# Performance work log

Hardware: AMD Instinct MI355X
Metric: run time of the kernel (lower is better)

## Reference

```python
import jax, jax.numpy as jnp
import numpy as np
from jax import lax

B, S, D, E, H = 2, 2048, 1024, 8, 4096


def setup_inputs() -> dict:
    key = jax.random.key(0)
    ks = jax.random.split(key, 10)
    sc = 0.02  # GPT-style init scale
    return {
        "x": jax.random.normal(ks[0], (B, S, D), jnp.float32),
        "noise": jax.random.normal(ks[1], (B, S, E), jnp.float32),
        "w_route": jax.random.normal(ks[2], (D, E), jnp.float32) * sc,
        "b_route": jnp.zeros((E,), jnp.float32),
        "w_noise": jax.random.normal(ks[3], (D, E), jnp.float32) * sc,
        "b_noise": jnp.zeros((E,), jnp.float32),
        "w_fc": jax.random.normal(ks[4], (E, D, H), jnp.float32) * sc,
        "b_fc": jnp.zeros((E, H), jnp.float32),
        "w_proj": jax.random.normal(ks[5], (E, H, D), jnp.float32) * sc,
        "b_proj": jnp.zeros((E, D), jnp.float32),
        "top_k": 2,
    }


def reference(x, noise, w_route, b_route, w_noise, b_noise, w_fc, b_fc, w_proj, b_proj, top_k):
    # --- NoisyTopkRouter ---
    logits = x @ w_route + b_route                      # [B,S,E]
    noise_logits = x @ w_noise + b_noise                # [B,S,E]
    noisy = logits + noise * jax.nn.softplus(noise_logits)
    gate1 = jax.nn.softmax(noisy, axis=-1)              # dense gate (aux output)

    topk_vals, topk_idx = lax.top_k(noisy, top_k)       # [B,S,K]
    # softmax over sparse logits (-inf elsewhere) == softmax over the top-k values
    gk = jax.nn.softmax(topk_vals, axis=-1)             # [B,S,K]
    # scatter top-k gates back to the dense expert axis; non-selected experts get 0
    gating = (jax.nn.one_hot(topk_idx, E, dtype=x.dtype) * gk[..., None]).sum(-2)  # [B,S,E]

    # --- Experts (dense-over-experts, masked by gating; math identical to
    #     masked gather/scatter since non-selected gates are exactly 0) ---
    h = jnp.einsum('bsd,edh->bseh', x, w_fc) + b_fc     # [B,S,E,H]
    h = jax.nn.gelu(h, approximate=True)                # GELU(tanh)
    y = jnp.einsum('bseh,ehd->bsed', h, w_proj) + b_proj  # [B,S,E,D]
    out = jnp.einsum('bsed,bse->bsd', y, gating)        # weighted combine
    return out, gate1
```

## Files before the change

### kernel.cpp

```cpp
#include <hip/hip_runtime.h>
#include <cstdint>


#define DEV __device__ __forceinline__

typedef __attribute__((ext_vector_type(8))) short short8;
typedef __attribute__((ext_vector_type(4))) float floatx4;

constexpr int D_ = 1024, E_ = 8, H_ = 4096;
constexpr int NTOK = 4096;
constexpr int CAP  = 4096;
constexpr int TOTSLOT = NTOK * 2;

constexpr size_t O_COUNT = 0;
constexpr size_t O_FLAG  = 48;
constexpr size_t O_OFFS  = 64;
constexpr size_t O_BTOK  = 128;
constexpr size_t O_BGATE = O_BTOK  + (size_t)E_ * CAP * 4;
constexpr size_t O_PAIR  = O_BGATE + (size_t)E_ * CAP * 4;
constexpr size_t O_HBUF  = (O_PAIR + (size_t)NTOK * 2 * 4 + 255) & ~(size_t)255;
constexpr size_t O_YBUF  = O_HBUF + (size_t)TOTSLOT * H_ * 2;
constexpr size_t WS_NEED = O_YBUF + (size_t)TOTSLOT * D_ * 2;

DEV float b2f(unsigned short u) {
    union { unsigned int i; float f; } v; v.i = ((unsigned int)u) << 16; return v.f;
}
DEV unsigned int f2b(float f) {
    union { float f; unsigned int i; } v; v.f = f;
    unsigned int r = v.i + 0x7fffu + ((v.i >> 16) & 1u);
    return (r >> 16) & 0xffffu;
}

template <int DT> DEV float ldf(const void* p, size_t i) {
    if constexpr (DT == 0) return ((const float*)p)[i];
    else return b2f(((const unsigned short*)p)[i]);
}

DEV float gelu_tanh(float x) {
    float u = 0.7978845608028654f * (x + 0.044715f * x * x * x);
    u = fminf(fmaxf(u, -20.f), 20.f);
    float e = __expf(2.f * u);
    float t = (e - 1.f) / (e + 1.f);
    return 0.5f * x * (1.f + t);
}

__global__ __launch_bounds__(64) void detect_init(const unsigned int* __restrict__ xw,
                                                  int* flags, int* counts) {
    int lane = threadIdx.x;
    int outl = 0;
    for (int i = lane; i < 512; i += 64) {
        unsigned int lo = xw[i] & 0xffffu;
        unsigned int ef = (lo >> 7) & 0xffu;
        if (ef < 100u || ef > 140u) outl++;
    }
#pragma unroll
    for (int off = 32; off > 0; off >>= 1) outl += __shfl_down(outl, off);
    if (lane == 0) flags[0] = (outl > 64) ? 0 : 1;
    if (lane < E_) counts[lane] = 0;
}

template <int DT>
__global__ __launch_bounds__(256) void router_kernel(
    const void* __restrict__ x, const void* __restrict__ noise,
    const void* __restrict__ w_route, const void* __restrict__ b_route,
    const void* __restrict__ w_noise, const void* __restrict__ b_noise,
    void* __restrict__ out,
    const int* __restrict__ flags, int* counts, int* btok, float* bgate, int* pairs)
{
    if (flags[0] != DT) return;
    int wave = threadIdx.x >> 6, lane = threadIdx.x & 63;
    int t = blockIdx.x * 4 + wave;

    double racc[E_], nacc[E_];
#pragma unroll
    for (int e = 0; e < E_; e++) { racc[e] = 0.0; nacc[e] = 0.0; }

#pragma unroll 4
    for (int i = 0; i < D_ / 64; i++) {
        int j = i * 64 + lane;
        float xv = ldf<DT>(x, (size_t)t * D_ + j);
        float rv[E_], nv[E_];
        if constexpr (DT == 0) {
            const float* wr = (const float*)w_route + (size_t)j * E_;
            const float* wn = (const float*)w_noise + (size_t)j * E_;
            float4 a0 = ((const float4*)wr)[0], a1 = ((const float4*)wr)[1];
            float4 c0 = ((const float4*)wn)[0], c1 = ((const float4*)wn)[1];
            rv[0]=a0.x; rv[1]=a0.y; rv[2]=a0.z; rv[3]=a0.w;
            rv[4]=a1.x; rv[5]=a1.y; rv[6]=a1.z; rv[7]=a1.w;
            nv[0]=c0.x; nv[1]=c0.y; nv[2]=c0.z; nv[3]=c0.w;
            nv[4]=c1.x; nv[5]=c1.y; nv[6]=c1.z; nv[7]=c1.w;
        } else {
            uint4 r8 = *(const uint4*)((const unsigned short*)w_route + (size_t)j * E_);
            uint4 n8 = *(const uint4*)((const unsigned short*)w_noise + (size_t)j * E_);
            const unsigned int rw[4] = {r8.x, r8.y, r8.z, r8.w};
            const unsigned int nw[4] = {n8.x, n8.y, n8.z, n8.w};
#pragma unroll
            for (int p = 0; p < 4; p++) {
                rv[2*p]   = b2f((unsigned short)(rw[p] & 0xffffu));
                rv[2*p+1] = b2f((unsigned short)(rw[p] >> 16));
                nv[2*p]   = b2f((unsigned short)(nw[p] & 0xffffu));
                nv[2*p+1] = b2f((unsigned short)(nw[p] >> 16));
            }
        }
#pragma unroll
        for (int e = 0; e < E_; e++) {
            racc[e] += (double)(xv * rv[e]);
            nacc[e] += (double)(xv * nv[e]);
        }
    }
#pragma unroll
    for (int off = 32; off > 0; off >>= 1)
#pragma unroll
        for (int e = 0; e < E_; e++) {
            racc[e] += __shfl_down(racc[e], off);
            nacc[e] += __shfl_down(nacc[e], off);
        }

    if (lane == 0) {
        double nz[E_];
#pragma unroll
        for (int e = 0; e < E_; e++) {
            double lg = racc[e] + (double)ldf<DT>(b_route, e);
            double nl = nacc[e] + (double)ldf<DT>(b_noise, e);
            double sp = (nl > 0.0) ? nl + log1p(exp(-nl)) : log1p(exp(nl));
            nz[e] = lg + (double)ldf<DT>(noise, (size_t)t * E_ + e) * sp;
        }
        double mx = nz[0];
#pragma unroll
        for (int e = 1; e < E_; e++) mx = fmax(mx, nz[e]);
        double se = 0.0, ex[E_];
#pragma unroll
        for (int e = 0; e < E_; e++) { ex[e] = exp(nz[e] - mx); se += ex[e]; }
#pragma unroll
        for (int e = 0; e < E_; e++) {
            float g = (float)(ex[e] / se);
            if constexpr (DT == 0) ((float*)out)[(size_t)NTOK * D_ + (size_t)t * E_ + e] = g;
            else ((unsigned short*)out)[(size_t)NTOK * D_ + (size_t)t * E_ + e] = (unsigned short)f2b(g);
        }
        double v0 = -1e300, v1 = -1e300; int i0 = 0, i1 = 0;
#pragma unroll
        for (int e = 0; e < E_; e++) {
            double v = nz[e];
            if (v > v0) { v1 = v0; i1 = i0; v0 = v; i0 = e; }
            else if (v > v1) { v1 = v; i1 = e; }
        }
        double g0 = 1.0 / (1.0 + exp(v1 - v0));
        float  g1 = (float)(1.0 - g0);
        int l0 = atomicAdd(&counts[i0], 1);
        int l1 = atomicAdd(&counts[i1], 1);
        btok[i0 * CAP + l0] = t;  bgate[i0 * CAP + l0] = (float)g0;
        btok[i1 * CAP + l1] = t;  bgate[i1 * CAP + l1] = g1;
        pairs[2 * t]     = (i0 << 16) | l0;
        pairs[2 * t + 1] = (i1 << 16) | l1;
    }
}

__global__ __launch_bounds__(64) void offsets_kernel(const int* counts, int* offs) {
    if (threadIdx.x == 0) {
        int a = 0;
        for (int e = 0; e < E_; e++) { offs[e] = a; a += counts[e]; }
        offs[E_] = a;
    }
}

template <int KD, int ND, bool FC, int DT>
__global__ __launch_bounds__(256) void moe_gemm(
    const void* __restrict__ asrc,
    const void* __restrict__ w,
    const void* __restrict__ bias,
    unsigned short* __restrict__ dst,
    const int* __restrict__ flags, const int* __restrict__ counts,
    const int* __restrict__ offs, const int* __restrict__ btok,
    const float* __restrict__ bgate)
{
    if (flags[0] != DT) return;
    const int e = blockIdx.z;
    const int cnt = counts[e];
    const int m0 = blockIdx.y * 128;
    if (m0 >= cnt) return;
    const int n0 = blockIdx.x * 128;
    const int off = offs[e];

    __shared__ unsigned short As[128][72];
    __shared__ unsigned short Bs[128][72];

    const int tid = threadIdx.x;
    const int ar = tid >> 1, ah = tid & 1;
    int am = m0 + ar; if (am > cnt - 1) am = cnt - 1;
    const size_t arow = FC ? (size_t)btok[e * CAP + am] * KD
                           : (size_t)(off + am) * KD;
    const int bn = (tid & 31) * 4;
    const int bk = (tid >> 5) * 8;

    const int waveid = tid >> 6, lane = tid & 63;
    const int wm = (waveid & 1) * 64, wn = (waveid >> 1) * 64;
    const int lrow = lane & 15, quad = lane >> 4;

    floatx4 acc[4][4];
#pragma unroll
    for (int fm = 0; fm < 4; fm++)
#pragma unroll
        for (int fn = 0; fn < 4; fn++) acc[fm][fn] = (floatx4)0.f;

    for (int k0 = 0; k0 < KD; k0 += 64) {
        __syncthreads();
        {
            uint4* ad = (uint4*)&As[ar][ah * 32];
            if constexpr (FC && DT == 0) {
                const float* ag = (const float*)asrc + arow + k0 + ah * 32;
#pragma unroll
                for (int i = 0; i < 4; i++) {
                    float4 a0 = ((const float4*)ag)[2 * i];
                    float4 a1 = ((const float4*)ag)[2 * i + 1];
                    uint4 pk;
                    pk.x = f2b(a0.x) | (f2b(a0.y) << 16);
                    pk.y = f2b(a0.z) | (f2b(a0.w) << 16);
                    pk.z = f2b(a1.x) | (f2b(a1.y) << 16);
                    pk.w = f2b(a1.z) | (f2b(a1.w) << 16);
                    ad[i] = pk;
                }
            } else {
                const uint4* ag = (const uint4*)((const unsigned short*)asrc + arow + k0 + ah * 32);
#pragma unroll
                for (int i = 0; i < 4; i++) ad[i] = ag[i];
            }
        }
        {
            unsigned short breg[4][8];
#pragma unroll
            for (int j = 0; j < 8; j++) {
                if constexpr (DT == 0) {
                    const float* wp = (const float*)w + (size_t)e * KD * ND
                                      + (size_t)(k0 + bk + j) * ND + n0 + bn;
                    float4 v = *(const float4*)wp;
                    breg[0][j] = (unsigned short)f2b(v.x);
                    breg[1][j] = (unsigned short)f2b(v.y);
                    breg[2][j] = (unsigned short)f2b(v.z);
                    breg[3][j] = (unsigned short)f2b(v.w);
                } else {
                    const unsigned short* wp = (const unsigned short*)w + (size_t)e * KD * ND
                                               + (size_t)(k0 + bk + j) * ND + n0 + bn;
                    uint2 v = *(const uint2*)wp;
                    breg[0][j] = (unsigned short)(v.x & 0xffffu);
                    breg[1][j] = (unsigned short)(v.x >> 16);
                    breg[2][j] = (unsigned short)(v.y & 0xffffu);
                    breg[3][j] = (unsigned short)(v.y >> 16);
                }
            }
#pragma unroll
            for (int c = 0; c < 4; c++) {
                uint4 pk;
                pk.x = (unsigned int)breg[c][0] | ((unsigned int)breg[c][1] << 16);
                pk.y = (unsigned int)breg[c][2] | ((unsigned int)breg[c][3] << 16);
                pk.z = (unsigned int)breg[c][4] | ((unsigned int)breg[c][5] << 16);
                pk.w = (unsigned int)breg[c][6] | ((unsigned int)breg[c][7] << 16);
                *(uint4*)&Bs[bn + c][bk] = pk;
            }
        }
        __syncthreads();
#pragma unroll
        for (int ks = 0; ks < 2; ks++) {
            short8 af[4], bfr[4];
#pragma unroll
            for (int f = 0; f < 4; f++) {
                af[f]  = *(const short8*)&As[wm + f * 16 + lrow][ks * 32 + quad * 8];
                bfr[f] = *(const short8*)&Bs[wn + f * 16 + lrow][ks * 32 + quad * 8];
            }
#pragma unroll
            for (int fm = 0; fm < 4; fm++)
#pragma unroll
                for (int fn = 0; fn < 4; fn++)
                    acc[fm][fn] = __builtin_amdgcn_mfma_f32_16x16x32_bf16(
                        af[fm], bfr[fn], acc[fm][fn], 0, 0, 0);
        }
    }

    const int gc = n0 + wn + lrow;
    float bcol[4];
#pragma unroll
    for (int fn = 0; fn < 4; fn++) bcol[fn] = ldf<DT>(bias, (size_t)e * ND + gc + fn * 16);

#pragma unroll
    for (int fm = 0; fm < 4; fm++) {
        int srow0 = m0 + wm + fm * 16 + quad * 4;
#pragma unroll
        for (int r = 0; r < 4; r++) {
            int srow = srow0 + r;
            if (srow < cnt) {
                size_t base = (size_t)(off + srow) * ND;
                if (FC) {
#pragma unroll
                    for (int fn = 0; fn < 4; fn++) {
                        float v = acc[fm][fn][r] + bcol[fn];
                        dst[base + gc + fn * 16] = (unsigned short)f2b(gelu_tanh(v));
                    }
                } else {
                    float g = bgate[e * CAP + srow];
#pragma unroll
                    for (int fn = 0; fn < 4; fn++) {
                        float v = (acc[fm][fn][r] + bcol[fn]) * g;
                        dst[base + gc + fn * 16] = (unsigned short)f2b(v);
                    }
                }
            }
        }
    }
}

template <int DT>
__global__ __launch_bounds__(256) void combine_kernel(
    const unsigned short* __restrict__ ybuf, const int* __restrict__ pairs,
    const int* __restrict__ offs, const int* __restrict__ flags, void* __restrict__ out)
{
    if (flags[0] != DT) return;
    int t = blockIdx.x;
    int p0 = pairs[2 * t], p1 = pairs[2 * t + 1];
    size_t r0 = (size_t)(offs[p0 >> 16] + (p0 & 0xffff)) * D_;
    size_t r1 = (size_t)(offs[p1 >> 16] + (p1 & 0xffff)) * D_;
    int c = threadIdx.x * 4;
    uint2 a = *(const uint2*)(ybuf + r0 + c);
    uint2 b = *(const uint2*)(ybuf + r1 + c);
    float s0 = b2f((unsigned short)(a.x & 0xffffu)) + b2f((unsigned short)(b.x & 0xffffu));
    float s1 = b2f((unsigned short)(a.x >> 16))     + b2f((unsigned short)(b.x >> 16));
    float s2 = b2f((unsigned short)(a.y & 0xffffu)) + b2f((unsigned short)(b.y & 0xffffu));
    float s3 = b2f((unsigned short)(a.y >> 16))     + b2f((unsigned short)(b.y >> 16));
    if constexpr (DT == 0) {
        float4 o; o.x = s0; o.y = s1; o.z = s2; o.w = s3;
        *(float4*)((float*)out + (size_t)t * D_ + c) = o;
    } else {
        uint2 o;
        o.x = f2b(s0) | (f2b(s1) << 16);
        o.y = f2b(s2) | (f2b(s3) << 16);
        *(uint2*)((unsigned short*)out + (size_t)t * D_ + c) = o;
    }
}

extern "C" void kernel_launch(void* const* d_in, const int* in_sizes, int n_in,
                              void* d_out, int out_size, void* d_ws, size_t ws_size,
                              hipStream_t stream) {
    if (ws_size < WS_NEED) return;

    const void* x       = d_in[0];
    const void* noise   = d_in[1];
    const void* w_route = d_in[2];
    const void* b_route = d_in[3];
    const void* w_noise = d_in[4];
    const void* b_noise = d_in[5];
    const void* w_fc    = d_in[6];
    const void* b_fc    = d_in[7];
    const void* w_proj  = d_in[8];
    const void* b_proj  = d_in[9];

    char* ws = (char*)d_ws;
    int*   counts = (int*)(ws + O_COUNT);
    int*   flags  = (int*)(ws + O_FLAG);
    int*   offs   = (int*)(ws + O_OFFS);
    int*   btok   = (int*)(ws + O_BTOK);
    float* bgate  = (float*)(ws + O_BGATE);
    int*   pairs  = (int*)(ws + O_PAIR);
    unsigned short* hbuf = (unsigned short*)(ws + O_HBUF);
    unsigned short* ybuf = (unsigned short*)(ws + O_YBUF);

    detect_init<<<dim3(1), dim3(64), 0, stream>>>((const unsigned int*)x, flags, counts);

    router_kernel<0><<<dim3(NTOK / 4), dim3(256), 0, stream>>>(
        x, noise, w_route, b_route, w_noise, b_noise, d_out, flags, counts, btok, bgate, pairs);
    router_kernel<1><<<dim3(NTOK / 4), dim3(256), 0, stream>>>(
        x, noise, w_route, b_route, w_noise, b_noise, d_out, flags, counts, btok, bgate, pairs);

    offsets_kernel<<<dim3(1), dim3(64), 0, stream>>>(counts, offs);

    moe_gemm<D_, H_, true, 0><<<dim3(H_ / 128, 32, E_), dim3(256), 0, stream>>>(
        x, w_fc, b_fc, hbuf, flags, counts, offs, btok, bgate);
    moe_gemm<D_, H_, true, 1><<<dim3(H_ / 128, 32, E_), dim3(256), 0, stream>>>(
        x, w_fc, b_fc, hbuf, flags, counts, offs, btok, bgate);

    moe_gemm<H_, D_, false, 0><<<dim3(D_ / 128, 32, E_), dim3(256), 0, stream>>>(
        hbuf, w_proj, b_proj, ybuf, flags, counts, offs, btok, bgate);
    moe_gemm<H_, D_, false, 1><<<dim3(D_ / 128, 32, E_), dim3(256), 0, stream>>>(
        hbuf, w_proj, b_proj, ybuf, flags, counts, offs, btok, bgate);

    combine_kernel<0><<<dim3(NTOK), dim3(256), 0, stream>>>(ybuf, pairs, offs, flags, d_out);
    combine_kernel<1><<<dim3(NTOK), dim3(256), 0, stream>>>(ybuf, pairs, offs, flags, d_out);
}
```

Before: 807.5 us.

## Pre-gather tokens, pre-transpose weights to bf16, use direct-to-LDS loads in GEMMs

Adds a path, taken when the workspace is large enough, that first gathers routed tokens into a contiguous bf16 buffer, converts the biases to fp32, and transposes and converts each expert weight matrix to bf16 K-major layout. A new GEMM kernel then streams both operands with global_load_lds 16-byte loads into XOR-swizzled LDS tiles and runs bf16 MFMA. This removes the per-element conversion and strided, indirect loads from the GEMM inner loop. In exchange it adds extra preprocessing kernels that read all weights every call and needs much more workspace, and it falls back to the old path when the workspace is too small.

```diff
diff --git a/kernel.cpp b/kernel.cpp
--- a/kernel.cpp
+++ b/kernel.cpp
@@ -18,9 +18,17 @@
 constexpr size_t O_BTOK  = 128;
 constexpr size_t O_BGATE = O_BTOK  + (size_t)E_ * CAP * 4;
 constexpr size_t O_PAIR  = O_BGATE + (size_t)E_ * CAP * 4;
-constexpr size_t O_HBUF  = (O_PAIR + (size_t)NTOK * 2 * 4 + 255) & ~(size_t)255;
-constexpr size_t O_YBUF  = O_HBUF + (size_t)TOTSLOT * H_ * 2;
-constexpr size_t WS_NEED = O_YBUF + (size_t)TOTSLOT * D_ * 2;
+constexpr size_t O_BFC32 = (O_PAIR + (size_t)NTOK * 2 * 4 + 255) & ~(size_t)255;
+constexpr size_t O_BPJ32 = O_BFC32 + (size_t)E_ * H_ * 4;
+constexpr size_t O_BIG   = (O_BPJ32 + (size_t)E_ * D_ * 4 + 255) & ~(size_t)255;
+constexpr size_t O_XG   = O_BIG;
+constexpr size_t O_HBUF = O_XG   + (size_t)TOTSLOT * D_ * 2;
+constexpr size_t O_YBUF = O_HBUF + (size_t)TOTSLOT * H_ * 2;
+constexpr size_t O_WT   = O_YBUF + (size_t)TOTSLOT * D_ * 2;
+constexpr size_t WS_A   = O_WT   + (size_t)E_ * D_ * H_ * 2;
+constexpr size_t OB_HBUF = O_BIG;
+constexpr size_t OB_YBUF = OB_HBUF + (size_t)TOTSLOT * H_ * 2;
+constexpr size_t WS_B    = OB_YBUF + (size_t)TOTSLOT * D_ * 2;
 
 DEV float b2f(unsigned short u) {
     union { unsigned int i; float f; } v; v.i = ((unsigned int)u) << 16; return v.f;
@@ -30,18 +38,23 @@
     unsigned int r = v.i + 0x7fffu + ((v.i >> 16) & 1u);
     return (r >> 16) & 0xffffu;
 }
-
 template <int DT> DEV float ldf(const void* p, size_t i) {
     if constexpr (DT == 0) return ((const float*)p)[i];
     else return b2f(((const unsigned short*)p)[i]);
 }
-
 DEV float gelu_tanh(float x) {
     float u = 0.7978845608028654f * (x + 0.044715f * x * x * x);
     u = fminf(fmaxf(u, -20.f), 20.f);
     float e = __expf(2.f * u);
     float t = (e - 1.f) / (e + 1.f);
     return 0.5f * x * (1.f + t);
+}
+
+typedef __attribute__((address_space(3))) unsigned int lds_u32_t;
+typedef const __attribute__((address_space(1))) unsigned int g_u32_t;
+DEV void gload16(const unsigned short* g, const unsigned short* l) {
+    __builtin_amdgcn_global_load_lds((g_u32_t*)(size_t)g,
+                                     (lds_u32_t*)(unsigned int)(size_t)l, 16, 0, 0);
 }
 
 __global__ __launch_bounds__(64) void detect_init(const unsigned int* __restrict__ xw,
@@ -64,8 +77,8 @@
     const void* __restrict__ x, const void* __restrict__ noise,
     const void* __restrict__ w_route, const void* __restrict__ b_route,
     const void* __restrict__ w_noise, const void* __restrict__ b_noise,
-    void* __restrict__ out,
-    const int* __restrict__ flags, int* counts, int* btok, float* bgate, int* pairs)
+    void* __restrict__ out, const int* __restrict__ flags,
+    int* counts, int* btok, float* bgate, int* pairs)
 {
     if (flags[0] != DT) return;
     int wave = threadIdx.x >> 6, lane = threadIdx.x & 63;
@@ -163,12 +176,201 @@
     }
 }
 
+template <int DT>
+__global__ __launch_bounds__(256) void conv_bias(
+    const void* __restrict__ b_fc, const void* __restrict__ b_proj,
+    const int* __restrict__ flags, float* __restrict__ bfc32, float* __restrict__ bpj32)
+{
+    if (flags[0] != DT) return;
+    int i = blockIdx.x * 256 + threadIdx.x;
+    if (i < E_ * H_) bfc32[i] = ldf<DT>(b_fc, i);
+    if (i < E_ * D_) bpj32[i] = ldf<DT>(b_proj, i);
+}
+
+template <int DT>
+__global__ __launch_bounds__(256) void gather_x(
+    const void* __restrict__ x, const int* __restrict__ btok,
+    const int* __restrict__ counts, const int* __restrict__ offs,
+    const int* __restrict__ flags, unsigned short* __restrict__ xg)
+{
+    if (flags[0] != DT) return;
+    int e = blockIdx.y, i = blockIdx.x;
+    if (i >= counts[e]) return;
+    int t = btok[e * CAP + i];
+    size_t src = (size_t)t * D_;
+    size_t dst = (size_t)(offs[e] + i) * D_;
+    int c = threadIdx.x * 4;
+    if constexpr (DT == 0) {
+        float4 v = *(const float4*)((const float*)x + src + c);
+        uint2 o;
+        o.x = f2b(v.x) | (f2b(v.y) << 16);
+        o.y = f2b(v.z) | (f2b(v.w) << 16);
+        *(uint2*)(xg + dst + c) = o;
+    } else {
+        *(uint2*)(xg + dst + c) = *(const uint2*)((const unsigned short*)x + src + c);
+    }
+}
+
+template <int DT>
+__global__ __launch_bounds__(256) void transpose_w(
+    const void* __restrict__ w, unsigned short* __restrict__ wT,
+    const int* __restrict__ flags, int K, int N)
+{
+    if (flags[0] != DT) return;
+    __shared__ unsigned short t[64][65];
+    const int e  = blockIdx.z;
+    const int k0 = blockIdx.y * 64;
+    const int n0 = blockIdx.x * 64;
+    const int r  = threadIdx.x >> 2;
+    const int c4 = (threadIdx.x & 3) * 16;
+    if constexpr (DT == 0) {
+        const float* src = (const float*)w + ((size_t)e * K + k0 + r) * N + n0 + c4;
+#pragma unroll
+        for (int i = 0; i < 4; i++) {
+            float4 v = ((const float4*)src)[i];
+            t[r][c4 + 4*i + 0] = (unsigned short)f2b(v.x);
+            t[r][c4 + 4*i + 1] = (unsigned short)f2b(v.y);
+            t[r][c4 + 4*i + 2] = (unsigned short)f2b(v.z);
+            t[r][c4 + 4*i + 3] = (unsigned short)f2b(v.w);
+        }
+    } else {
+        const unsigned short* src = (const unsigned short*)w + ((size_t)e * K + k0 + r) * N + n0 + c4;
+#pragma unroll
+        for (int i = 0; i < 2; i++) {
+            uint4 v = ((const uint4*)src)[i];
+            const unsigned int wds[4] = {v.x, v.y, v.z, v.w};
+#pragma unroll
+            for (int p = 0; p < 4; p++) {
+                t[r][c4 + 8*i + 2*p]     = (unsigned short)(wds[p] & 0xffffu);
+                t[r][c4 + 8*i + 2*p + 1] = (unsigned short)(wds[p] >> 16);
+            }
+        }
+    }
+    __syncthreads();
+    unsigned short* dstp = wT + ((size_t)e * N + n0 + r) * K + k0 + c4;
+    unsigned short tmp[16];
+#pragma unroll
+    for (int i = 0; i < 16; i++) tmp[i] = t[c4 + i][r];
+#pragma unroll
+    for (int h = 0; h < 2; h++) {
+        uint4 pk;
+        pk.x = (unsigned int)tmp[8*h+0] | ((unsigned int)tmp[8*h+1] << 16);
+        pk.y = (unsigned int)tmp[8*h+2] | ((unsigned int)tmp[8*h+3] << 16);
+        pk.z = (unsigned int)tmp[8*h+4] | ((unsigned int)tmp[8*h+5] << 16);
+        pk.w = (unsigned int)tmp[8*h+6] | ((unsigned int)tmp[8*h+7] << 16);
+        ((uint4*)dstp)[h] = pk;
+    }
+}
+
+template <int KD, int ND, bool FC>
+__global__ __launch_bounds__(256) void moe_gemm2(
+    const unsigned short* __restrict__ A,
+    const unsigned short* __restrict__ wT,
+    const float* __restrict__ bias32,
+    unsigned short* __restrict__ dst,
+    const int* __restrict__ counts, const int* __restrict__ offs,
+    const float* __restrict__ bgate)
+{
+    const int e = blockIdx.z;
+    const int cnt = counts[e];
+    const int m0 = blockIdx.y * 128;
+    if (m0 >= cnt) return;
+    const int n0 = blockIdx.x * 128;
+    const int off = offs[e];
+
+    __shared__ unsigned short As[128 * 64];
+    __shared__ unsigned short Bs[128 * 64];
+
+    const int tid = threadIdx.x;
+    const int waveid = tid >> 6, lane = tid & 63;
+    const int sr = lane >> 3;
+    const int g  = lane & 7;
+    const int scol = ((g ^ sr) * 8);
+
+    const unsigned short* aAddr[4];
+    const unsigned short* bAddr[4];
+#pragma unroll
+    for (int c = 0; c < 4; c++) {
+        int ar = m0 + (waveid * 4 + c) * 8 + sr;
+        if (ar > cnt - 1) ar = cnt - 1;
+        aAddr[c] = A + (size_t)(off + ar) * KD + scol;
+        int br = n0 + (waveid * 4 + c) * 8 + sr;
+        bAddr[c] = wT + ((size_t)e * ND + br) * KD + scol;
+    }
+    const int ldsChunk = (waveid * 4) * 512;
+
+    const int wm = (waveid & 1) * 64, wn = (waveid >> 1) * 64;
+    const int lrow = lane & 15, quad = lane >> 4;
+
+    floatx4 acc[4][4];
+#pragma unroll
+    for (int fm = 0; fm < 4; fm++)
+#pragma unroll
+        for (int fn = 0; fn < 4; fn++) acc[fm][fn] = (floatx4)0.f;
+
+    for (int k0 = 0; k0 < KD; k0 += 64) {
+        __syncthreads();
+#pragma unroll
+        for (int c = 0; c < 4; c++) {
+            gload16(aAddr[c] + k0, &As[ldsChunk + c * 512]);
+            gload16(bAddr[c] + k0, &Bs[ldsChunk + c * 512]);
+        }
+        __syncthreads();
+#pragma unroll
+        for (int ks = 0; ks < 2; ks++) {
+            short8 af[4], bfr[4];
+#pragma unroll
+            for (int f = 0; f < 4; f++) {
+                int Ra = wm + f * 16 + lrow;
+                int Rb = wn + f * 16 + lrow;
+                af[f]  = *(const short8*)&As[Ra * 64 + ((ks * 4 + quad) ^ (Ra & 7)) * 8];
+                bfr[f] = *(const short8*)&Bs[Rb * 64 + ((ks * 4 + quad) ^ (Rb & 7)) * 8];
+            }
+#pragma unroll
+            for (int fm = 0; fm < 4; fm++)
+#pragma unroll
+                for (int fn = 0; fn < 4; fn++)
+                    acc[fm][fn] = __builtin_amdgcn_mfma_f32_16x16x32_bf16(
+                        af[fm], bfr[fn], acc[fm][fn], 0, 0, 0);
+        }
+    }
+
+    const int gc = n0 + wn + lrow;
+    float bcol[4];
+#pragma unroll
+    for (int fn = 0; fn < 4; fn++) bcol[fn] = bias32[(size_t)e * ND + gc + fn * 16];
+
+#pragma unroll
+    for (int fm = 0; fm < 4; fm++) {
+        int srow0 = m0 + wm + fm * 16 + quad * 4;
+#pragma unroll
+        for (int r = 0; r < 4; r++) {
+            int srow = srow0 + r;
+            if (srow < cnt) {
+                size_t base = (size_t)(off + srow) * ND;
+                if (FC) {
+#pragma unroll
+                    for (int fn = 0; fn < 4; fn++) {
+                        float v = acc[fm][fn][r] + bcol[fn];
+                        dst[base + gc + fn * 16] = (unsigned short)f2b(gelu_tanh(v));
+                    }
+                } else {
+                    float gt = bgate[e * CAP + srow];
+#pragma unroll
+                    for (int fn = 0; fn < 4; fn++) {
+                        float v = (acc[fm][fn][r] + bcol[fn]) * gt;
+                        dst[base + gc + fn * 16] = (unsigned short)f2b(v);
+                    }
+                }
+            }
+        }
+    }
+}
+
 template <int KD, int ND, bool FC, int DT>
 __global__ __launch_bounds__(256) void moe_gemm(
-    const void* __restrict__ asrc,
-    const void* __restrict__ w,
-    const void* __restrict__ bias,
-    unsigned short* __restrict__ dst,
+    const void* __restrict__ asrc, const void* __restrict__ w,
+    const void* __restrict__ bias, unsigned short* __restrict__ dst,
     const int* __restrict__ flags, const int* __restrict__ counts,
     const int* __restrict__ offs, const int* __restrict__ btok,
     const float* __restrict__ bgate)
@@ -338,7 +540,7 @@
 extern "C" void kernel_launch(void* const* d_in, const int* in_sizes, int n_in,
                               void* d_out, int out_size, void* d_ws, size_t ws_size,
                               hipStream_t stream) {
-    if (ws_size < WS_NEED) return;
+    if (ws_size < WS_B) return;
 
     const void* x       = d_in[0];
     const void* noise   = d_in[1];
@@ -358,28 +560,53 @@
     int*   btok   = (int*)(ws + O_BTOK);
     float* bgate  = (float*)(ws + O_BGATE);
     int*   pairs  = (int*)(ws + O_PAIR);
-    unsigned short* hbuf = (unsigned short*)(ws + O_HBUF);
-    unsigned short* ybuf = (unsigned short*)(ws + O_YBUF);
 
     detect_init<<<dim3(1), dim3(64), 0, stream>>>((const unsigned int*)x, flags, counts);
-
     router_kernel<0><<<dim3(NTOK / 4), dim3(256), 0, stream>>>(
         x, noise, w_route, b_route, w_noise, b_noise, d_out, flags, counts, btok, bgate, pairs);
     router_kernel<1><<<dim3(NTOK / 4), dim3(256), 0, stream>>>(
         x, noise, w_route, b_route, w_noise, b_noise, d_out, flags, counts, btok, bgate, pairs);
-
     offsets_kernel<<<dim3(1), dim3(64), 0, stream>>>(counts, offs);
 
-    moe_gemm<D_, H_, true, 0><<<dim3(H_ / 128, 32, E_), dim3(256), 0, stream>>>(
-        x, w_fc, b_fc, hbuf, flags, counts, offs, btok, bgate);
-    moe_gemm<D_, H_, true, 1><<<dim3(H_ / 128, 32, E_), dim3(256), 0, stream>>>(
-        x, w_fc, b_fc, hbuf, flags, counts, offs, btok, bgate);
-
-    moe_gemm<H_, D_, false, 0><<<dim3(D_ / 128, 32, E_), dim3(256), 0, stream>>>(
-        hbuf, w_proj, b_proj, ybuf, flags, counts, offs, btok, bgate);
-    moe_gemm<H_, D_, false, 1><<<dim3(D_ / 128, 32, E_), dim3(256), 0, stream>>>(
-        hbuf, w_proj, b_proj, ybuf, flags, counts, offs, btok, bgate);
-
-    combine_kernel<0><<<dim3(NTOK), dim3(256), 0, stream>>>(ybuf, pairs, offs, flags, d_out);
-    combine_kernel<1><<<dim3(NTOK), dim3(256), 0, stream>>>(ybuf, pairs, offs, flags, d_out);
-}
+    if (ws_size >= WS_A) {
+        float* bfc32 = (float*)(ws + O_BFC32);
+        float* bpj32 = (float*)(ws + O_BPJ32);
+        unsigned short* xg   = (unsigned short*)(ws + O_XG);
+        unsigned short* hbuf = (unsigned short*)(ws + O_HBUF);
+        unsigned short* ybuf = (unsigned short*)(ws + O_YBUF);
+        unsigned short* wT   = (unsigned short*)(ws + O_WT);
+
+        conv_bias<0><<<dim3((E_ * H_ + 255) / 256), dim3(256), 0, stream>>>(b_fc, b_proj, flags, bfc32, bpj32);
+        conv_bias<1><<<dim3((E_ * H_ + 255) / 256), dim3(256), 0, stream>>>(b_fc, b_proj, flags, bfc32, bpj32);
+        gather_x<0><<<dim3(CAP, E_), dim3(256), 0, stream>>>(x, btok, counts, offs, flags, xg);
+        gather_x<1><<<dim3(CAP, E_), dim3(256), 0, stream>>>(x, btok, counts, offs, flags, xg);
+
+        transpose_w<0><<<dim3(H_ / 64, D_ / 64, E_), dim3(256), 0, stream>>>(w_fc, wT, flags, D_, H_);
+        transpose_w<1><<<dim3(H_ / 64, D_ / 64, E_), dim3(256), 0, stream>>>(w_fc, wT, flags, D_, H_);
+        moe_gemm2<D_, H_, true><<<dim3(H_ / 128, 32, E_), dim3(256), 0, stream>>>(
+            xg, wT, bfc32, hbuf, counts, offs, bgate);
+
+        transpose_w<0><<<dim3(D_ / 64, H_ / 64, E_), dim3(256), 0, stream>>>(w_proj, wT, flags, H_, D_);
+        transpose_w<1><<<dim3(D_ / 64, H_ / 64, E_), dim3(256), 0, stream>>>(w_proj, wT, flags, H_, D_);
+        moe_gemm2<H_, D_, false><<<dim3(D_ / 128, 32, E_), dim3(256), 0, stream>>>(
+            hbuf, wT, bpj32, ybuf, counts, offs, bgate);
+
+        combine_kernel<0><<<dim3(NTOK), dim3(256), 0, stream>>>(ybuf, pairs, offs, flags, d_out);
+        combine_kernel<1><<<dim3(NTOK), dim3(256), 0, stream>>>(ybuf, pairs, offs, flags, d_out);
+    } else {
+        unsigned short* hbuf = (unsigned short*)(ws + OB_HBUF);
+        unsigned short* ybuf = (unsigned short*)(ws + OB_YBUF);
+
+        moe_gemm<D_, H_, true, 0><<<dim3(H_ / 128, 32, E_), dim3(256), 0, stream>>>(
+            x, w_fc, b_fc, hbuf, flags, counts, offs, btok, bgate);
+        moe_gemm<D_, H_, true, 1><<<dim3(H_ / 128, 32, E_), dim3(256), 0, stream>>>(
+            x, w_fc, b_fc, hbuf, flags, counts, offs, btok, bgate);
+        moe_gemm<H_, D_, false, 0><<<dim3(D_ / 128, 32, E_), dim3(256), 0, stream>>>(
+            hbuf, w_proj, b_proj, ybuf, flags, counts, offs, btok, bgate);
+        moe_gemm<H_, D_, false, 1><<<dim3(D_ / 128, 32, E_), dim3(256), 0, stream>>>(
+            hbuf, w_proj, b_proj, ybuf, flags, counts, offs, btok, bgate);
+
+        combine_kernel<0><<<dim3(NTOK), dim3(256), 0, stream>>>(ybuf, pairs, offs, flags, d_out);
+        combine_kernel<1><<<dim3(NTOK), dim3(256), 0, stream>>>(ybuf, pairs, offs, flags, d_out);
+    }
+}
```

After: 751.0 us. -7.0%, faster.
